# Kernel tuning notes

Hardware: AMD Instinct MI355X
Metric: run time of the kernel (lower is better)

The kernel has to match this reference:

```python
import jax, jax.numpy as jnp
import numpy as np

NUM_HEADS = 32
NUM_KV_HEADS = 8
HEAD_DIM = 128
SCALE = 0.08838834764831845  # 1/sqrt(HEAD_DIM)
SEQ_LEN = 2048
NEG_INF = -1e30


def setup_inputs() -> dict:
    key = jax.random.key(0)
    k1, k2, k3 = jax.random.split(key, 3)
    query = jax.random.normal(k1, (SEQ_LEN, NUM_HEADS * HEAD_DIM), dtype=jnp.float32)
    key_t = jax.random.normal(k2, (SEQ_LEN, NUM_KV_HEADS * HEAD_DIM), dtype=jnp.float32)
    value = jax.random.normal(k3, (SEQ_LEN, NUM_KV_HEADS * HEAD_DIM), dtype=jnp.float32)
    return {"query": query, "key": key_t, "value": value}


def reference(query, key, value):
    S = query.shape[0]
    n_rep = NUM_HEADS // NUM_KV_HEADS
    # GQA: group q heads by kv head instead of materializing repeated K/V.
    q = query.reshape(S, NUM_KV_HEADS, n_rep, HEAD_DIM)   # [S, G, R, D]
    k = key.reshape(S, NUM_KV_HEADS, HEAD_DIM)            # [S, G, D]
    v = value.reshape(S, NUM_KV_HEADS, HEAD_DIM)          # [S, G, D]
    # scores: [G, R, S(query), S(key)]
    scores = jnp.einsum('sgrd,tgd->grst', q, k) * jnp.float32(SCALE)
    # causal mask (prefill: seq_len > 1 -> is_causal=True)
    causal = jnp.arange(S)[:, None] >= jnp.arange(S)[None, :]  # [S, S]
    scores = jnp.where(causal, scores, NEG_INF)
    probs = jax.nn.softmax(scores, axis=-1)
    out = jnp.einsum('grst,tgd->sgrd', probs, v)          # [S, G, R, D]
    return out.reshape(S, NUM_HEADS * HEAD_DIM)
```

## Files before the change

kernel.cpp:

```cpp
#include <hip/hip_runtime.h>


#define SEQ    2048
#define NH     32
#define NKV    8
#define DHEAD  128
#define QROW   (NH * DHEAD)
#define KVROW  (NKV * DHEAD)
#define SCALE  0.08838834764831845f
#define LOG2E  1.4426950408889634f
#define BN     64
#define VSTRP  132

typedef __attribute__((ext_vector_type(8))) short bf16x8;
typedef __attribute__((ext_vector_type(8))) unsigned short u16x8;
typedef __attribute__((ext_vector_type(4))) float f32x4;

static __device__ __forceinline__ unsigned short f2bf(float f) {
  unsigned int u = __float_as_uint(f);
  return (unsigned short)((u + 0x7fffu + ((u >> 16) & 1u)) >> 16);
}
static __device__ __forceinline__ unsigned short f2bf_fast(float f) {
  return (unsigned short)((__float_as_uint(f) + 0x8000u) >> 16);
}

#define DPP_F(x, ctrl) \
  __int_as_float(__builtin_amdgcn_mov_dpp(__float_as_int(x), (ctrl), 0xf, 0xf, true))
static __device__ __forceinline__ float red16_sum(float x) {
  x += DPP_F(x, 0xB1);
  x += DPP_F(x, 0x4E);
  x += DPP_F(x, 0x141);
  x += DPP_F(x, 0x140);
  return x;
}

__global__ __launch_bounds__(256) void prep_kernel(
    const float* __restrict__ K, const float* __restrict__ V,
    unsigned short* __restrict__ Kg, unsigned short* __restrict__ VTg) {
  __shared__ unsigned short Vs[64 * VSTRP];
  const int t0  = blockIdx.x * 64;
  const int g   = blockIdx.y;
  const int tid = threadIdx.x;
  for (int e = 0; e < 8; ++e) {
    int fi = e * 256 + tid;
    int t  = fi >> 5;
    int c4 = fi & 31;
    const float4 kv = *(const float4*)(K + (size_t)(t0 + t) * KVROW + g * DHEAD + c4 * 4);
    ushort4 kb = {f2bf(kv.x), f2bf(kv.y), f2bf(kv.z), f2bf(kv.w)};
    *(ushort4*)(Kg + ((size_t)(g * SEQ + t0 + t) << 7) + c4 * 4) = kb;
    const float4 vv = *(const float4*)(V + (size_t)(t0 + t) * KVROW + g * DHEAD + c4 * 4);
    ushort4 vb = {f2bf(vv.x), f2bf(vv.y), f2bf(vv.z), f2bf(vv.w)};
    *(ushort4*)&Vs[t * VSTRP + c4 * 4] = vb;
  }
  __syncthreads();
  for (int e = 0; e < 4; ++e) {
    int idx = e * 256 + tid;
    int d  = idx >> 3;
    int tb = idx & 7;
    u16x8 o;
    for (int j = 0; j < 8; ++j) o[j] = Vs[(tb * 8 + j) * VSTRP + d];
    *(u16x8*)(VTg + (size_t)(g * DHEAD + d) * SEQ + t0 + tb * 8) = o;
  }
}

static __device__ __forceinline__ void stage_kv(
    const unsigned short* __restrict__ Kg, const unsigned short* __restrict__ VTg,
    unsigned short* kbuf, unsigned short* vbuf, int g, int kt, int w, int lane) {
  const int t0 = kt * BN;
  for (int c = 0; c < 2; ++c) {
    int off = (w * 2 + c) * 512 + lane * 8;
    int tl  = off >> 7;
    int dsw = (off & 127) ^ (8 * (tl & 7));
    const unsigned short* src = Kg + ((size_t)(g * SEQ + t0 + tl) << 7) + dsw;
    __builtin_amdgcn_global_load_lds(
        (const __attribute__((address_space(1))) void*)src,
        (__attribute__((address_space(3))) void*)(kbuf + (w * 2 + c) * 512), 16, 0, 0);
  }
  for (int c = 0; c < 2; ++c) {
    int off = (w * 2 + c) * 512 + lane * 8;
    int dl  = off >> 6;
    int tsw = (off & 63) ^ (8 * (dl & 7));
    const unsigned short* src = VTg + (size_t)(g * DHEAD + dl) * SEQ + t0 + tsw;
    __builtin_amdgcn_global_load_lds(
        (const __attribute__((address_space(1))) void*)src,
        (__attribute__((address_space(3))) void*)(vbuf + (w * 2 + c) * 512), 16, 0, 0);
  }
}

__global__ __launch_bounds__(512, 4) void sdpa_fa8_kernel(
    const float* __restrict__ Q, float* __restrict__ O,
    const unsigned short* __restrict__ Kg, const unsigned short* __restrict__ VTg) {
  __shared__ unsigned short Kb[2][BN * DHEAD];
  __shared__ unsigned short Vb[2][DHEAD * BN];
  __shared__ unsigned short Ps[8][16 * 64];

  const int b  = blockIdx.x;
  const int g  = b & 7;
  const int q5 = (b >> 3) & 31;
  const int jj = (b >= 256) ? q5 : 63 - q5;
  const int q0 = jj * 32;
  const int nt = (jj >> 1) + 1;
  const int tid  = threadIdx.x;
  const int w    = tid >> 6;
  const int lane = tid & 63;
  const int quad = lane >> 4;
  const int l16  = lane & 15;
  const int h    = g * 4 + (w & 3);
  const int r0   = q0 + (w >> 2) * 16;
  const int sw   = 8 * (l16 & 7);

  bf16x8 qf[4];
  {
    const float* qrow = Q + (size_t)(r0 + l16) * QROW + h * DHEAD;
    for (int kc = 0; kc < 4; ++kc) {
      const float* p = qrow + kc * 32 + quad * 8;
      bf16x8 v;
      for (int j = 0; j < 8; ++j) v[j] = (short)f2bf(p[j] * (SCALE * LOG2E));
      qf[kc] = v;
    }
  }

  f32x4 oacc[8];
  for (int i = 0; i < 8; ++i) oacc[i] = (f32x4){0.f, 0.f, 0.f, 0.f};
  float lsum[4] = {0.f, 0.f, 0.f, 0.f};

  unsigned short* pw = &Ps[w][0];

  stage_kv(Kg, VTg, Kb[0], Vb[0], g, 0, w, lane);
  __syncthreads();

  for (int kt = 0; kt < nt; ++kt) {
    const int cur = kt & 1;
    if (kt + 1 < nt)
      stage_kv(Kg, VTg, Kb[cur ^ 1], Vb[cur ^ 1], g, kt + 1, w, lane);

    const bool diag = (kt == nt - 1);

    for (int nb = 0; nb < 4; ++nb) {
      f32x4 sacc = (f32x4){0.f, 0.f, 0.f, 0.f};
      for (int kc = 0; kc < 4; ++kc) {
        bf16x8 kf = *(const bf16x8*)&Kb[cur][(nb * 16 + l16) * DHEAD + ((kc * 32 + quad * 8) ^ sw)];
        sacc = __builtin_amdgcn_mfma_f32_16x16x32_bf16(qf[kc], kf, sacc, 0, 0, 0);
      }
      for (int r = 0; r < 4; ++r) {
        float x = sacc[r];
        if (diag) {
          int tg = kt * BN + nb * 16 + l16;
          int rg = r0 + quad * 4 + r;
          x = (tg > rg) ? -1e30f : x;
        }
        float p = __builtin_amdgcn_exp2f(x);
        lsum[r] += p;
        int qr = quad * 4 + r;
        pw[qr * 64 + ((nb * 16 + l16) ^ (8 * (qr & 7)))] = f2bf_fast(p);
      }
    }

    bf16x8 pa[2];
    for (int kc = 0; kc < 2; ++kc)
      pa[kc] = *(const bf16x8*)&pw[l16 * 64 + ((kc * 32 + quad * 8) ^ sw)];

    for (int nb2 = 0; nb2 < 8; ++nb2)
      for (int kc = 0; kc < 2; ++kc) {
        bf16x8 vf = *(const bf16x8*)&Vb[cur][(nb2 * 16 + l16) * BN + ((kc * 32 + quad * 8) ^ sw)];
        oacc[nb2] = __builtin_amdgcn_mfma_f32_16x16x32_bf16(pa[kc], vf, oacc[nb2], 0, 0, 0);
      }

    __syncthreads();
  }

  for (int r = 0; r < 4; ++r) {
    float inv = 1.f / red16_sum(lsum[r]);
    float* orow = O + (size_t)(r0 + quad * 4 + r) * QROW + h * DHEAD;
    for (int nb2 = 0; nb2 < 8; ++nb2)
      orow[nb2 * 16 + l16] = oacc[nb2][r] * inv;
  }
}

extern "C" void kernel_launch(void* const* d_in, const int* in_sizes, int n_in,
                              void* d_out, int out_size, void* d_ws, size_t ws_size,
                              hipStream_t stream) {
  (void)in_sizes; (void)n_in; (void)out_size; (void)ws_size;
  const float* Q = (const float*)d_in[0];
  const float* K = (const float*)d_in[1];
  const float* V = (const float*)d_in[2];
  float* O = (float*)d_out;
  unsigned short* Kg  = (unsigned short*)d_ws;
  unsigned short* VTg = Kg + (size_t)NKV * SEQ * DHEAD;
  prep_kernel<<<dim3(SEQ / 64, NKV), 256, 0, stream>>>(K, V, Kg, VTg);
  sdpa_fa8_kernel<<<512, 512, 0, stream>>>(Q, O, Kg, VTg);
}
```

Measured before the change: 151.2 us.

## Switch attention to 32x32 MFMA with register-resident P and 4-wave blocks

```diff
diff --git a/kernel.cpp b/kernel.cpp
--- a/kernel.cpp
+++ b/kernel.cpp
@@ -14,50 +14,52 @@
 
 typedef __attribute__((ext_vector_type(8))) short bf16x8;
 typedef __attribute__((ext_vector_type(8))) unsigned short u16x8;
-typedef __attribute__((ext_vector_type(4))) float f32x4;
+typedef __attribute__((ext_vector_type(16))) float f32x16;
+typedef __attribute__((ext_vector_type(4))) unsigned int u32x4;
 
 static __device__ __forceinline__ unsigned short f2bf(float f) {
   unsigned int u = __float_as_uint(f);
   return (unsigned short)((u + 0x7fffu + ((u >> 16) & 1u)) >> 16);
 }
-static __device__ __forceinline__ unsigned short f2bf_fast(float f) {
-  return (unsigned short)((__float_as_uint(f) + 0x8000u) >> 16);
-}
-
-#define DPP_F(x, ctrl) \
-  __int_as_float(__builtin_amdgcn_mov_dpp(__float_as_int(x), (ctrl), 0xf, 0xf, true))
-static __device__ __forceinline__ float red16_sum(float x) {
-  x += DPP_F(x, 0xB1);
-  x += DPP_F(x, 0x4E);
-  x += DPP_F(x, 0x141);
-  x += DPP_F(x, 0x140);
-  return x;
+
+static __device__ __forceinline__ unsigned cvtpk_bf16(float lo, float hi) {
+  unsigned r;
+  asm("v_cvt_pk_bf16_f32 %0, %1, %2" : "=v"(r) : "v"(lo), "v"(hi));
+  return r;
+}
+
+static __device__ __forceinline__ f32x16 zero16() {
+  f32x16 z;
+#pragma unroll
+  for (int i = 0; i < 16; ++i) z[i] = 0.f;
+  return z;
 }
 
 __global__ __launch_bounds__(256) void prep_kernel(
     const float* __restrict__ K, const float* __restrict__ V,
     unsigned short* __restrict__ Kg, unsigned short* __restrict__ VTg) {
-  __shared__ unsigned short Vs[64 * VSTRP];
-  const int t0  = blockIdx.x * 64;
+  __shared__ unsigned short Vs[16 * VSTRP];
+  const int t0  = blockIdx.x * 16;
   const int g   = blockIdx.y;
   const int tid = threadIdx.x;
-  for (int e = 0; e < 8; ++e) {
+#pragma unroll
+  for (int e = 0; e < 2; ++e) {
     int fi = e * 256 + tid;
     int t  = fi >> 5;
     int c4 = fi & 31;
     const float4 kv = *(const float4*)(K + (size_t)(t0 + t) * KVROW + g * DHEAD + c4 * 4);
-    ushort4 kb = {f2bf(kv.x), f2bf(kv.y), f2bf(kv.z), f2bf(kv.w)};
-    *(ushort4*)(Kg + ((size_t)(g * SEQ + t0 + t) << 7) + c4 * 4) = kb;
+    ushort4 kb4 = {f2bf(kv.x), f2bf(kv.y), f2bf(kv.z), f2bf(kv.w)};
+    *(ushort4*)(Kg + ((size_t)(g * SEQ + t0 + t) << 7) + c4 * 4) = kb4;
     const float4 vv = *(const float4*)(V + (size_t)(t0 + t) * KVROW + g * DHEAD + c4 * 4);
-    ushort4 vb = {f2bf(vv.x), f2bf(vv.y), f2bf(vv.z), f2bf(vv.w)};
-    *(ushort4*)&Vs[t * VSTRP + c4 * 4] = vb;
+    ushort4 vb4 = {f2bf(vv.x), f2bf(vv.y), f2bf(vv.z), f2bf(vv.w)};
+    *(ushort4*)&Vs[t * VSTRP + c4 * 4] = vb4;
   }
   __syncthreads();
-  for (int e = 0; e < 4; ++e) {
-    int idx = e * 256 + tid;
-    int d  = idx >> 3;
-    int tb = idx & 7;
+  {
+    int d  = tid >> 1;
+    int tb = tid & 1;
     u16x8 o;
+#pragma unroll
     for (int j = 0; j < 8; ++j) o[j] = Vs[(tb * 8 + j) * VSTRP + d];
     *(u16x8*)(VTg + (size_t)(g * DHEAD + d) * SEQ + t0 + tb * 8) = o;
   }
@@ -67,64 +69,91 @@
     const unsigned short* __restrict__ Kg, const unsigned short* __restrict__ VTg,
     unsigned short* kbuf, unsigned short* vbuf, int g, int kt, int w, int lane) {
   const int t0 = kt * BN;
-  for (int c = 0; c < 2; ++c) {
-    int off = (w * 2 + c) * 512 + lane * 8;
+#pragma unroll
+  for (int c = 0; c < 4; ++c) {
+    int off = (w * 4 + c) * 512 + lane * 8;
     int tl  = off >> 7;
-    int dsw = (off & 127) ^ (8 * (tl & 7));
+    int dsw = (off & 127) ^ (8 * (tl & 15));
     const unsigned short* src = Kg + ((size_t)(g * SEQ + t0 + tl) << 7) + dsw;
     __builtin_amdgcn_global_load_lds(
         (const __attribute__((address_space(1))) void*)src,
-        (__attribute__((address_space(3))) void*)(kbuf + (w * 2 + c) * 512), 16, 0, 0);
-  }
-  for (int c = 0; c < 2; ++c) {
-    int off = (w * 2 + c) * 512 + lane * 8;
+        (__attribute__((address_space(3))) void*)(kbuf + (w * 4 + c) * 512), 16, 0, 0);
+  }
+#pragma unroll
+  for (int c = 0; c < 4; ++c) {
+    int off = (w * 4 + c) * 512 + lane * 8;
     int dl  = off >> 6;
     int tsw = (off & 63) ^ (8 * (dl & 7));
     const unsigned short* src = VTg + (size_t)(g * DHEAD + dl) * SEQ + t0 + tsw;
     __builtin_amdgcn_global_load_lds(
         (const __attribute__((address_space(1))) void*)src,
-        (__attribute__((address_space(3))) void*)(vbuf + (w * 2 + c) * 512), 16, 0, 0);
-  }
-}
-
-__global__ __launch_bounds__(512, 4) void sdpa_fa8_kernel(
+        (__attribute__((address_space(3))) void*)(vbuf + (w * 4 + c) * 512), 16, 0, 0);
+  }
+}
+
+#define PV_KSTEP(PP, S, KS2)                                                     \
+  do {                                                                           \
+    unsigned y0 = cvtpk_bf16((PP)[(2 * (S)) * 4 + 0], (PP)[(2 * (S)) * 4 + 1]);  \
+    unsigned z0 = cvtpk_bf16((PP)[(2 * (S)) * 4 + 2], (PP)[(2 * (S)) * 4 + 3]);  \
+    unsigned y1 = cvtpk_bf16((PP)[(2 * (S) + 1) * 4 + 0], (PP)[(2 * (S) + 1) * 4 + 1]); \
+    unsigned z1 = cvtpk_bf16((PP)[(2 * (S) + 1) * 4 + 2], (PP)[(2 * (S) + 1) * 4 + 3]); \
+    asm("v_permlane32_swap_b32 %0, %1" : "+v"(y0), "+v"(y1));                    \
+    asm("v_permlane32_swap_b32 %0, %1" : "+v"(z0), "+v"(z1));                    \
+    u32x4 paw = (u32x4){y0, z0, y1, z1};                                         \
+    bf16x8 pa = __builtin_bit_cast(bf16x8, paw);                                 \
+    const int tcol = (KS2) * 16 + hi * 8;                                        \
+    _Pragma("unroll")                                                            \
+    for (int nd = 0; nd < 4; ++nd) {                                             \
+      int drow = nd * 32 + l32;                                                  \
+      bf16x8 vf = *(const bf16x8*)&Vb[cur][drow * BN + (tcol ^ (8 * (drow & 7)))]; \
+      oacc[nd] = __builtin_amdgcn_mfma_f32_32x32x16_bf16(pa, vf, oacc[nd], 0, 0, 0); \
+    }                                                                            \
+  } while (0)
+
+__global__ __launch_bounds__(256, 2) void sdpa_w32_kernel(
     const float* __restrict__ Q, float* __restrict__ O,
     const unsigned short* __restrict__ Kg, const unsigned short* __restrict__ VTg) {
   __shared__ unsigned short Kb[2][BN * DHEAD];
   __shared__ unsigned short Vb[2][DHEAD * BN];
-  __shared__ unsigned short Ps[8][16 * 64];
-
-  const int b  = blockIdx.x;
-  const int g  = b & 7;
-  const int q5 = (b >> 3) & 31;
-  const int jj = (b >= 256) ? q5 : 63 - q5;
-  const int q0 = jj * 32;
-  const int nt = (jj >> 1) + 1;
-  const int tid  = threadIdx.x;
-  const int w    = tid >> 6;
+  __shared__ float Ls[4][32];
+
+  const int b   = blockIdx.x;
+  const int g   = b & 7;
+  const int q5  = (b >> 3) & 31;
+  const int jj  = (b >= 256) ? q5 : 63 - q5;
+  const int q0  = jj * 32;
+  const int nt  = (jj >> 1) + 1;
+  const int tid = threadIdx.x;
+  const int w   = tid >> 6;
   const int lane = tid & 63;
-  const int quad = lane >> 4;
-  const int l16  = lane & 15;
-  const int h    = g * 4 + (w & 3);
-  const int r0   = q0 + (w >> 2) * 16;
-  const int sw   = 8 * (l16 & 7);
-
-  bf16x8 qf[4];
+  const int l32 = lane & 31;
+  const int hi  = lane >> 5;
+  const int h   = g * 4 + w;
+
+  bf16x8 qf[8];
   {
-    const float* qrow = Q + (size_t)(r0 + l16) * QROW + h * DHEAD;
-    for (int kc = 0; kc < 4; ++kc) {
-      const float* p = qrow + kc * 32 + quad * 8;
+    const float* qp = Q + (size_t)(q0 + l32) * QROW + h * DHEAD + hi * 8;
+#pragma unroll
+    for (int ks = 0; ks < 8; ++ks) {
+      const float4 a = *(const float4*)(qp + ks * 16);
+      const float4 c = *(const float4*)(qp + ks * 16 + 4);
       bf16x8 v;
-      for (int j = 0; j < 8; ++j) v[j] = (short)f2bf(p[j] * (SCALE * LOG2E));
-      qf[kc] = v;
-    }
-  }
-
-  f32x4 oacc[8];
-  for (int i = 0; i < 8; ++i) oacc[i] = (f32x4){0.f, 0.f, 0.f, 0.f};
-  float lsum[4] = {0.f, 0.f, 0.f, 0.f};
-
-  unsigned short* pw = &Ps[w][0];
+      v[0] = (short)f2bf(a.x * (SCALE * LOG2E));
+      v[1] = (short)f2bf(a.y * (SCALE * LOG2E));
+      v[2] = (short)f2bf(a.z * (SCALE * LOG2E));
+      v[3] = (short)f2bf(a.w * (SCALE * LOG2E));
+      v[4] = (short)f2bf(c.x * (SCALE * LOG2E));
+      v[5] = (short)f2bf(c.y * (SCALE * LOG2E));
+      v[6] = (short)f2bf(c.z * (SCALE * LOG2E));
+      v[7] = (short)f2bf(c.w * (SCALE * LOG2E));
+      qf[ks] = v;
+    }
+  }
+
+  f32x16 oacc[4];
+#pragma unroll
+  for (int i = 0; i < 4; ++i) oacc[i] = zero16();
+  float lsum = 0.f;
 
   stage_kv(Kg, VTg, Kb[0], Vb[0], g, 0, w, lane);
   __syncthreads();
@@ -135,45 +164,70 @@
       stage_kv(Kg, VTg, Kb[cur ^ 1], Vb[cur ^ 1], g, kt + 1, w, lane);
 
     const bool diag = (kt == nt - 1);
-
-    for (int nb = 0; nb < 4; ++nb) {
-      f32x4 sacc = (f32x4){0.f, 0.f, 0.f, 0.f};
-      for (int kc = 0; kc < 4; ++kc) {
-        bf16x8 kf = *(const bf16x8*)&Kb[cur][(nb * 16 + l16) * DHEAD + ((kc * 32 + quad * 8) ^ sw)];
-        sacc = __builtin_amdgcn_mfma_f32_16x16x32_bf16(qf[kc], kf, sacc, 0, 0, 0);
+    const int KB = (diag && !(jj & 1)) ? 1 : 2;
+
+    f32x16 s0 = zero16();
+    f32x16 s1 = zero16();
+#pragma unroll
+    for (int ks = 0; ks < 8; ++ks) {
+      const int t = l32;
+      bf16x8 kf = *(const bf16x8*)&Kb[cur][t * DHEAD + (((ks * 16 + hi * 8)) ^ (8 * (t & 15)))];
+      s0 = __builtin_amdgcn_mfma_f32_32x32x16_bf16(kf, qf[ks], s0, 0, 0, 0);
+    }
+    if (KB == 2) {
+#pragma unroll
+      for (int ks = 0; ks < 8; ++ks) {
+        const int t = 32 + l32;
+        bf16x8 kf = *(const bf16x8*)&Kb[cur][t * DHEAD + (((ks * 16 + hi * 8)) ^ (8 * (t & 15)))];
+        s1 = __builtin_amdgcn_mfma_f32_32x32x16_bf16(kf, qf[ks], s1, 0, 0, 0);
       }
-      for (int r = 0; r < 4; ++r) {
-        float x = sacc[r];
-        if (diag) {
-          int tg = kt * BN + nb * 16 + l16;
-          int rg = r0 + quad * 4 + r;
-          x = (tg > rg) ? -1e30f : x;
-        }
-        float p = __builtin_amdgcn_exp2f(x);
-        lsum[r] += p;
-        int qr = quad * 4 + r;
-        pw[qr * 64 + ((nb * 16 + l16) ^ (8 * (qr & 7)))] = f2bf_fast(p);
+    }
+
+    const int keyb = kt * BN;
+    f32x16 p0, p1;
+#pragma unroll
+    for (int r = 0; r < 16; ++r) {
+      const int ko = (r & 3) + 8 * (r >> 2) + 4 * hi;
+      float x = s0[r];
+      x = (diag && (keyb + ko > q0 + l32)) ? -1e30f : x;
+      float e = __builtin_amdgcn_exp2f(x);
+      p0[r] = e;
+      lsum += e;
+    }
+    if (KB == 2) {
+#pragma unroll
+      for (int r = 0; r < 16; ++r) {
+        const int ko = 32 + (r & 3) + 8 * (r >> 2) + 4 * hi;
+        float x = s1[r];
+        x = (diag && (keyb + ko > q0 + l32)) ? -1e30f : x;
+        float e = __builtin_amdgcn_exp2f(x);
+        p1[r] = e;
+        lsum += e;
       }
     }
 
-    bf16x8 pa[2];
-    for (int kc = 0; kc < 2; ++kc)
-      pa[kc] = *(const bf16x8*)&pw[l16 * 64 + ((kc * 32 + quad * 8) ^ sw)];
-
-    for (int nb2 = 0; nb2 < 8; ++nb2)
-      for (int kc = 0; kc < 2; ++kc) {
-        bf16x8 vf = *(const bf16x8*)&Vb[cur][(nb2 * 16 + l16) * BN + ((kc * 32 + quad * 8) ^ sw)];
-        oacc[nb2] = __builtin_amdgcn_mfma_f32_16x16x32_bf16(pa[kc], vf, oacc[nb2], 0, 0, 0);
-      }
+    PV_KSTEP(p0, 0, 0);
+    PV_KSTEP(p0, 1, 1);
+    if (KB == 2) {
+      PV_KSTEP(p1, 0, 2);
+      PV_KSTEP(p1, 1, 3);
+    }
 
     __syncthreads();
   }
 
-  for (int r = 0; r < 4; ++r) {
-    float inv = 1.f / red16_sum(lsum[r]);
-    float* orow = O + (size_t)(r0 + quad * 4 + r) * QROW + h * DHEAD;
-    for (int nb2 = 0; nb2 < 8; ++nb2)
-      orow[nb2 * 16 + l16] = oacc[nb2][r] * inv;
+  {
+    float tot = lsum + __shfl_xor(lsum, 32);
+    if (hi == 0) Ls[w][l32] = 1.f / tot;
+  }
+  __syncthreads();
+#pragma unroll
+  for (int nd = 0; nd < 4; ++nd) {
+#pragma unroll
+    for (int r = 0; r < 16; ++r) {
+      const int row = (r & 3) + 8 * (r >> 2) + 4 * hi;
+      O[(size_t)(q0 + row) * QROW + h * DHEAD + nd * 32 + l32] = oacc[nd][r] * Ls[w][row];
+    }
   }
 }
 
@@ -187,6 +241,6 @@
   float* O = (float*)d_out;
   unsigned short* Kg  = (unsigned short*)d_ws;
   unsigned short* VTg = Kg + (size_t)NKV * SEQ * DHEAD;
-  prep_kernel<<<dim3(SEQ / 64, NKV), 256, 0, stream>>>(K, V, Kg, VTg);
-  sdpa_fa8_kernel<<<512, 512, 0, stream>>>(Q, O, Kg, VTg);
-}
+  prep_kernel<<<dim3(SEQ / 16, NKV), 256, 0, stream>>>(K, V, Kg, VTg);
+  sdpa_w32_kernel<<<512, 256, 0, stream>>>(Q, O, Kg, VTg);
+}
```

Result: no change. 153.0 us (+1.2%).
